# Kernel tuning notes

Hardware: AMD Instinct MI355X
Metric: run time of the kernel (lower is better)

The kernel has to match this reference:

```python
import jax, jax.numpy as jnp
import numpy as np

H, DST, DCONV, EXP = 640, 16, 4, 2
DIN = H * EXP          # 1280
DTR = -(-H // 16)      # 40
EPS = 1e-6


def rmsnorm(x, w):
    rms = jnp.sqrt(jnp.mean(x * x, axis=-1, keepdims=True) + EPS)
    return x / rms * w


def bitlinear(x, w, nw):
    # RMSNorm -> ternary weight quant + int8 activation quant (STE)
    x = rmsnorm(x, nw)
    alpha = jnp.maximum(jnp.mean(jnp.abs(w)), 1e-10)
    wq = jnp.clip(jnp.round(w / alpha), -1.0, 1.0)
    wq = w + jax.lax.stop_gradient(wq - w)
    gamma = jnp.maximum(jnp.max(jnp.abs(x), axis=-1, keepdims=True), 1e-10)
    xq = jnp.clip(jnp.round(x * 127.0 / gamma), -128.0, 127.0)
    xq = x + jax.lax.stop_gradient(xq - x)
    return (xq @ wq.T) * (alpha * gamma / 127.0)


def causal_conv1d(x, cw, cb):
    # x: [B,L,D]; depthwise causal conv, kernel DCONV
    pad = DCONV - 1
    xp = jnp.pad(x, ((0, 0), (pad, 0), (0, 0)))
    L = x.shape[1]
    out = jnp.zeros_like(x)
    for k in range(DCONV):
        out = out + xp[:, pad - k:pad - k + L, :] * cw[:, k]
    return out + cb


def selective_scan(x, dt, B_mat, C_mat, A_log):
    # x,dt: [B,L,D]; B_mat,C_mat: [B,L,N]; A_log: [D,N]
    A = -jnp.exp(A_log)
    dA = jnp.exp(A[None, None] * dt[..., None])                 # [B,L,D,N]
    dBx = dt[..., None] * B_mat[:, :, None, :] * x[..., None]   # [B,L,D,N]
    dA_t = jnp.moveaxis(dA, 1, 0)
    dBx_t = jnp.moveaxis(dBx, 1, 0)
    C_t = jnp.moveaxis(C_mat, 1, 0)

    def step(h, inp):
        da, dbx, c = inp
        h = da * h + dbx
        y = jnp.sum(h * c[:, None, :], axis=-1)  # [B,D]
        return h, y

    h0 = jnp.zeros(x.shape[:1] + (x.shape[2], A_log.shape[1]), x.dtype)
    _, ys = jax.lax.scan(step, h0, (dA_t, dBx_t, C_t))
    return jnp.moveaxis(ys, 0, 1)  # [B,L,D]


def setup_inputs() -> dict:
    key = jax.random.key(0)
    ks = jax.random.split(key, 10)
    sc_in = 1.0 / np.sqrt(H)
    sc_din = 1.0 / np.sqrt(DIN)
    A = np.tile(np.arange(1, DST + 1, dtype=np.float32)[None, :], (DIN, 1))
    return {
        "x": jax.random.normal(ks[0], (2, 2048, H), jnp.float32),
        "norm_w": jnp.ones((H,), jnp.float32),
        "in_w": jax.random.normal(ks[1], (DIN * 2, H), jnp.float32) * sc_in,
        "in_nw": jnp.ones((H,), jnp.float32),
        "conv_w": jax.random.normal(ks[2], (DIN, DCONV), jnp.float32) * 0.1,
        "conv_b": jnp.zeros((DIN,), jnp.float32),
        "dtu_w": jax.random.normal(ks[3], (DTR, DIN), jnp.float32) * sc_din,
        "dtu_nw": jnp.ones((DIN,), jnp.float32),
        "dtd_w": jax.random.normal(ks[4], (DIN, DTR), jnp.float32) / np.sqrt(DTR),
        "dtd_b": jnp.zeros((DIN,), jnp.float32),
        "Bp_w": jax.random.normal(ks[5], (DST, DIN), jnp.float32) * sc_din,
        "Bp_nw": jnp.ones((DIN,), jnp.float32),
        "Cp_w": jax.random.normal(ks[6], (DST, DIN), jnp.float32) * sc_din,
        "Cp_nw": jnp.ones((DIN,), jnp.float32),
        "A_log": jnp.asarray(np.log(A)),
        "D": jnp.ones((DIN,), jnp.float32),
        "out_w": jax.random.normal(ks[7], (H, DIN), jnp.float32) * sc_din,
        "out_nw": jnp.ones((DIN,), jnp.float32),
    }


def reference(x, norm_w, in_w, in_nw, conv_w, conv_b, dtu_w, dtu_nw, dtd_w, dtd_b,
              Bp_w, Bp_nw, Cp_w, Cp_nw, A_log, D, out_w, out_nw):
    residual = x
    xn = rmsnorm(x, norm_w)
    xz = bitlinear(xn, in_w, in_nw)
    x_path, z = jnp.split(xz, 2, axis=-1)
    x_path = causal_conv1d(x_path, conv_w, conv_b)
    x_path = jax.nn.silu(x_path)
    dt = jax.nn.softplus(bitlinear(x_path, dtu_w, dtu_nw) @ dtd_w.T + dtd_b)
    B_mat = bitlinear(x_path, Bp_w, Bp_nw)
    C_mat = bitlinear(x_path, Cp_w, Cp_nw)
    y = selective_scan(x_path, dt, B_mat, C_mat, A_log)
    y = y + x_path * D
    y = y * jax.nn.silu(z)
    return bitlinear(y, out_w, out_nw) + residual
```

## Files before the change

kernel.cpp:

```cpp
#include <hip/hip_runtime.h>
#include <hip/hip_bf16.h>
#include <cmath>

#define NROWS 4096
#define H_    640
#define DIN_  1280
#define DXZ   2560
#define DTR_  40
#define DST_  16
#define LSEQ  2048
#define EPS_  1e-6f
#define NCH   64
#define CL    32
#define NDG   20
#define KSPLIT 8
#define KCH (DIN_ / KSPLIT)
#define LOG2E 1.4426950408889634f
#define RLOG2E 0.6931471805599453f

typedef __attribute__((ext_vector_type(8))) short short8;
typedef __attribute__((ext_vector_type(4))) float f32x4;
typedef unsigned short ushort_t;

__device__ __forceinline__ float bf2f(short u) {
    return __uint_as_float((unsigned)(unsigned short)u << 16);
}
__device__ __forceinline__ short f2bfs(float x) { return (short)(__float_as_uint(x) >> 16); }

#define GLD16(gp, lp) __builtin_amdgcn_global_load_lds( \
    (const __attribute__((address_space(1))) unsigned int*)(unsigned long long)(gp), \
    (__attribute__((address_space(3))) unsigned int*)(unsigned int)(unsigned long long)(lp), 16, 0, 0)

__device__ __forceinline__ float wave_sum64(float v) {
    v += __shfl_xor(v, 1);  v += __shfl_xor(v, 2);  v += __shfl_xor(v, 4);
    v += __shfl_xor(v, 8);  v += __shfl_xor(v, 16); v += __shfl_xor(v, 32);
    return v;
}
__device__ __forceinline__ float wave_max64(float v) {
    v = fmaxf(v, __shfl_xor(v, 1));  v = fmaxf(v, __shfl_xor(v, 2));
    v = fmaxf(v, __shfl_xor(v, 4));  v = fmaxf(v, __shfl_xor(v, 8));
    v = fmaxf(v, __shfl_xor(v, 16)); v = fmaxf(v, __shfl_xor(v, 32));
    return v;
}
__device__ __forceinline__ float block_sum4(float v, float* red4) {
    v = wave_sum64(v);
    if ((threadIdx.x & 63) == 0) red4[threadIdx.x >> 6] = v;
    __syncthreads();
    return (red4[0] + red4[1]) + (red4[2] + red4[3]);
}
__device__ __forceinline__ float block_max4(float v, float* red4) {
    v = wave_max64(v);
    if ((threadIdx.x & 63) == 0) red4[threadIdx.x >> 6] = v;
    __syncthreads();
    return fmaxf(fmaxf(red4[0], red4[1]), fmaxf(red4[2], red4[3]));
}
__device__ __forceinline__ float block_reduce_sum256(float v, float* red) {
    int tid = threadIdx.x;
    red[tid] = v; __syncthreads();
    for (int o = 128; o; o >>= 1) { if (tid < o) red[tid] += red[tid + o]; __syncthreads(); }
    float r = red[0]; __syncthreads();
    return r;
}

__global__ __launch_bounds__(256) void k_pre(const float* __restrict__ x,
                                             const float* __restrict__ norm_w,
                                             const float* __restrict__ in_nw,
                                             const float* __restrict__ w0, const float* __restrict__ w1,
                                             const float* __restrict__ w2, const float* __restrict__ w3,
                                             const float* __restrict__ w4,
                                             int n0, int n1, int n2, int n3, int n4,
                                             __hip_bfloat16* __restrict__ xq, float* __restrict__ gamma,
                                             float* __restrict__ partials,
                                             float* __restrict__ zacc ) {
    __shared__ float red[256];
    const int tid = threadIdx.x;
    if (blockIdx.x < NROWS) {
        const int r = blockIdx.x;
        const float* xr = x + (size_t)r * H_;
        const bool has2 = (tid < H_ - 512);
        float v0 = xr[tid], v1 = xr[tid + 256], v2 = has2 ? xr[tid + 512] : 0.f;
        float sum = block_sum4(v0 * v0 + v1 * v1 + v2 * v2, red);
        float r1 = 1.f / sqrtf(sum / H_ + EPS_);
        v0 *= r1 * norm_w[tid];
        v1 *= r1 * norm_w[tid + 256];
        if (has2) v2 *= r1 * norm_w[tid + 512];
        sum = block_sum4(v0 * v0 + v1 * v1 + v2 * v2, red + 4);
        float r2 = 1.f / sqrtf(sum / H_ + EPS_);
        v0 *= r2 * in_nw[tid];
        v1 *= r2 * in_nw[tid + 256];
        if (has2) v2 *= r2 * in_nw[tid + 512];
        float mx = fmaxf(fmaxf(fabsf(v0), fabsf(v1)), fabsf(v2));
        float g = fmaxf(block_max4(mx, red + 8), 1e-10f);
        if (tid == 0) gamma[r] = g;
        float s = 127.f / g;
        __hip_bfloat16* o = xq + (size_t)r * H_;
        o[tid]       = __float2bfloat16(fminf(fmaxf(rintf(v0 * s), -128.f), 127.f));
        o[tid + 256] = __float2bfloat16(fminf(fmaxf(rintf(v1 * s), -128.f), 127.f));
        if (has2) o[tid + 512] = __float2bfloat16(fminf(fmaxf(rintf(v2 * s), -128.f), 127.f));
    } else {
        const int flat = blockIdx.x - NROWS;
        for (int i = flat * 256 + tid; i < NROWS * 72; i += 1280 * 256) zacc[i] = 0.f;
        const int wi = flat >> 8, xb = flat & 255;
        const float* w = (wi == 0) ? w0 : (wi == 1) ? w1 : (wi == 2) ? w2 : (wi == 3) ? w3 : w4;
        const int n = (wi == 0) ? n0 : (wi == 1) ? n1 : (wi == 2) ? n2 : (wi == 3) ? n3 : n4;
        float s = 0.f;
        for (int i = xb * 256 + tid; i < n; i += 65536) s += fabsf(w[i]);
        float t = block_reduce_sum256(s, red);
        if (tid == 0) partials[wi * 256 + xb] = t;
    }
}

__global__ __launch_bounds__(256) void k_quant_build(const float* __restrict__ in_w,
                                                     const float* __restrict__ out_w,
                                                     const float* __restrict__ dtu_w,
                                                     const float* __restrict__ Bp_w,
                                                     const float* __restrict__ Cp_w,
                                                     const float* __restrict__ partials,
                                                     float* __restrict__ alphas,
                                                     __hip_bfloat16* __restrict__ q_in,
                                                     __hip_bfloat16* __restrict__ q_out,
                                                     ushort_t* __restrict__ wq_sk,
                                                     int n0, int n1, int n2, int n3, int n4) {
    __shared__ double dred[256];
    const int tid = threadIdx.x;
    auto calc_alpha = [&](int wi, int n) -> float {
        double s = (double)partials[wi * 256 + tid];
        dred[tid] = s; __syncthreads();
        for (int o = 128; o; o >>= 1) { if (tid < o) dred[tid] += dred[tid + o]; __syncthreads(); }
        float a = fmaxf((float)(dred[0] / (double)n), 1e-10f);
        __syncthreads();
        return a;
    };
    if (blockIdx.x < 6400) {
        float a = calc_alpha(0, n0);
        if (blockIdx.x == 0) {
            float a1 = calc_alpha(1, n1), a2 = calc_alpha(2, n2);
            float a3 = calc_alpha(3, n3), a4 = calc_alpha(4, n4);
            if (tid == 0) {
                alphas[0] = a; alphas[1] = a1; alphas[2] = a2; alphas[3] = a3; alphas[4] = a4;
            }
        }
        int i = blockIdx.x * 256 + tid;
        ((ushort_t*)q_in)[i] = (ushort_t)f2bfs(fminf(fmaxf(rintf(in_w[i] / a), -1.f), 1.f));
    } else if (blockIdx.x < 9600) {
        float a = calc_alpha(4, n4);
        int i = (blockIdx.x - 6400) * 256 + tid;
        ((ushort_t*)q_out)[i] = (ushort_t)f2bfs(fminf(fmaxf(rintf(out_w[i] / a), -1.f), 1.f));
    } else {
        float a1 = calc_alpha(1, n1), a2 = calc_alpha(2, n2), a3 = calc_alpha(3, n3);
        int idx = (blockIdx.x - 9600) * 256 + tid;
        int t = idx / 2560, rem = idx % 2560, kb = rem / 64, l = rem % 64;
        int nloc = l & 15, kg = l >> 4;
        float alpha; const float* src; int row; bool valid = true;
        if (t < 3)      { alpha = a1; src = dtu_w; row = t * 16 + nloc; valid = (row < 40); }
        else if (t == 3){ alpha = a2; src = Bp_w;  row = nloc; }
        else            { alpha = a3; src = Cp_w;  row = nloc; }
        int k0 = kb * 32 + kg * 8;
        short8 outv;
#pragma unroll
        for (int e = 0; e < 8; ++e) {
            float q = valid ? fminf(fmaxf(rintf(src[(size_t)row * DIN_ + k0 + e] / alpha), -1.f), 1.f) : 0.f;
            outv[e] = f2bfs(q);
        }
        *(short8*)(wq_sk + (size_t)idx * 8) = outv;
    }
}

template<int BM, int BN>
__global__ __launch_bounds__(256) void k_gemm_mfma(const ushort_t* __restrict__ Aq,
                                                   const ushort_t* __restrict__ Wq,
                                                   const float* __restrict__ alpha_p,
                                                   const float* __restrict__ gamma,
                                                   const float* __restrict__ residual,
                                                   float* __restrict__ out,
                                                   int M, int N, int K) {
    constexpr int FM = BM / 32, FN = BN / 32;
    constexpr int NL = (BM + BN) / 64;
    __shared__ ushort_t As[3][BM * 32];
    __shared__ ushort_t Bs[3][BN * 32];
    const int tid = threadIdx.x;
    const int w = tid >> 6, lane = tid & 63;
    const int wm = w >> 1, wn = w & 1;
    const int nwg = gridDim.x * gridDim.y;
    const int hw = blockIdx.y * gridDim.x + blockIdx.x;
    const int work = (nwg % 8 == 0) ? ((hw & 7) * (nwg >> 3) + (hw >> 3)) : hw;
    const int row0 = (work / gridDim.x) * BM;
    const int col0 = (work % gridDim.x) * BN;
    f32x4 acc[FM][FN] = {};

    auto stage = [&](int buf, int k0) {
        #pragma unroll
        for (int q = 0; q < BM / 64; ++q) {
            int c = w * BM + q * 64 + lane;
            int row = c >> 2;
            int uslot = (c & 3) ^ (row & 3);
            GLD16(Aq + (size_t)(row0 + row) * K + k0 + uslot * 8,
                  (char*)As[buf] + (w * BM + q * 64) * 16);
        }
        #pragma unroll
        for (int q = 0; q < BN / 64; ++q) {
            int c = w * BN + q * 64 + lane;
            int row = c >> 2;
            int uslot = (c & 3) ^ (row & 3);
            GLD16(Wq + (size_t)(col0 + row) * K + k0 + uslot * 8,
                  (char*)Bs[buf] + (w * BN + q * 64) * 16);
        }
    };

    const int NT = K >> 5;
    stage(0, 0);
    if (NT > 1) stage(1, 32);
    int cur = 0;
    for (int t = 0; t < NT; ++t) {
        if (t + 2 < NT) {
            int nb = cur + 2; if (nb >= 3) nb -= 3;
            stage(nb, (t + 2) << 5);
            if constexpr (NL == 2)      asm volatile("s_waitcnt vmcnt(4)" ::: "memory");
            else if constexpr (NL == 3) asm volatile("s_waitcnt vmcnt(6)" ::: "memory");
            else                        asm volatile("s_waitcnt vmcnt(8)" ::: "memory");
        } else if (t + 1 < NT) {
            if constexpr (NL == 2)      asm volatile("s_waitcnt vmcnt(2)" ::: "memory");
            else if constexpr (NL == 3) asm volatile("s_waitcnt vmcnt(3)" ::: "memory");
            else                        asm volatile("s_waitcnt vmcnt(4)" ::: "memory");
        } else {
            asm volatile("s_waitcnt vmcnt(0)" ::: "memory");
        }
        __builtin_amdgcn_s_barrier();

        short8 a[FM], b[FN];
        #pragma unroll
        for (int i = 0; i < FM; ++i) {
            int row = wm * (BM / 2) + i * 16 + (lane & 15);
            int byt = row * 64 + (((lane >> 4) ^ (row & 3)) << 4);
            a[i] = *(const short8*)((const char*)As[cur] + byt);
        }
        #pragma unroll
        for (int j = 0; j < FN; ++j) {
            int row = wn * (BN / 2) + j * 16 + (lane & 15);
            int byt = row * 64 + (((lane >> 4) ^ (row & 3)) << 4);
            b[j] = *(const short8*)((const char*)Bs[cur] + byt);
        }
        #pragma unroll
        for (int i = 0; i < FM; ++i)
            #pragma unroll
            for (int j = 0; j < FN; ++j)
                acc[i][j] = __builtin_amdgcn_mfma_f32_16x16x32_bf16(a[i], b[j], acc[i][j], 0, 0, 0);
        asm volatile("" ::: "memory");
        __builtin_amdgcn_s_barrier();
        ++cur; if (cur == 3) cur = 0;
    }

    const float alpha = alpha_p[0];
    #pragma unroll
    for (int i = 0; i < FM; ++i) {
        #pragma unroll
        for (int r = 0; r < 4; ++r) {
            int row = row0 + wm * (BM / 2) + i * 16 + (lane >> 4) * 4 + r;
            float s = alpha * gamma[row] * (1.f / 127.f);
            #pragma unroll
            for (int j = 0; j < FN; ++j) {
                int col = col0 + wn * (BN / 2) + j * 16 + (lane & 15);
                float o = acc[i][j][r] * s;
                if (residual) o += residual[(size_t)row * N + col];
                out[(size_t)row * N + col] = o;
            }
        }
    }
}

__global__ __launch_bounds__(256) void k_conv_norm(const float* __restrict__ xz,
                                                   const float* __restrict__ cw, const float* __restrict__ cb,
                                                   const float* __restrict__ dtu_nw,
                                                   const float* __restrict__ Bp_nw,
                                                   const float* __restrict__ Cp_nw,
                                                   float* __restrict__ xp,
                                                   float* __restrict__ rinv_out, float* __restrict__ g3) {
    const int bb = blockIdx.x;
    const int row = ((bb & 7) << 9) | (bb >> 3);
    const int tid = threadIdx.x;
    const int l = row & (LSEQ - 1);
    __shared__ float red4[16];
    float vv[5];
    float ss = 0.f;
#pragma unroll
    for (int j = 0; j < 5; ++j) {
        int d = tid + j * 256;
        f32x4 c4 = *(const f32x4*)(cw + (size_t)d * 4);
        const float* base = xz + (size_t)row * DXZ + d;
        float s = cb[d] + base[0] * c4[0];
        if (l >= 1) s += base[-(ptrdiff_t)DXZ] * c4[1];
        if (l >= 2) s += base[-(ptrdiff_t)(2 * DXZ)] * c4[2];
        if (l >= 3) s += base[-(ptrdiff_t)(3 * DXZ)] * c4[3];
        float v = s / (1.f + __builtin_amdgcn_exp2f(-s * LOG2E));
        vv[j] = v;
        ss += v * v;
        xp[(size_t)row * DIN_ + d] = v;
    }
    float sum = block_sum4(ss, red4);
    float rms = 1.f / sqrtf(sum / DIN_ + EPS_);
    float m0 = 0.f, m1 = 0.f, m2 = 0.f;
#pragma unroll
    for (int j = 0; j < 5; ++j) {
        int d = tid + j * 256;
        float t = vv[j] * rms;
        m0 = fmaxf(m0, fabsf(t * dtu_nw[d]));
        m1 = fmaxf(m1, fabsf(t * Bp_nw[d]));
        m2 = fmaxf(m2, fabsf(t * Cp_nw[d]));
    }
    float g0 = block_max4(m0, red4 + 4);
    float g1 = block_max4(m1, red4 + 8);
    float g2 = block_max4(m2, red4 + 12);
    if (tid == 0) {
        rinv_out[row]       = rms;
        g3[row]             = fmaxf(g0, 1e-10f);
        g3[NROWS + row]     = fmaxf(g1, 1e-10f);
        g3[2 * NROWS + row] = fmaxf(g2, 1e-10f);
    }
}

__global__ __launch_bounds__(256) void k_skinny_mfma(const float* __restrict__ xp,
                                                     const float* __restrict__ rinv,
                                                     const float* __restrict__ dtu_nw,
                                                     const float* __restrict__ Bp_nw,
                                                     const float* __restrict__ Cp_nw,
                                                     const float* __restrict__ g3,
                                                     const ushort_t* __restrict__ wq_sk,
                                                     float* __restrict__ dtu_acc,
                                                     float* __restrict__ B_acc,
                                                     float* __restrict__ C_acc) {
    const int tid = threadIdx.x;
    const int w = tid >> 6, l = tid & 63;
    const int row0 = blockIdx.x * 64;
    const int kc0 = blockIdx.y * KCH;
    __shared__ float s_xp[64 * 36];
    __shared__ float s_nw[3 * KCH];
    for (int i = tid; i < 3 * KCH; i += 256) {
        int m = i / KCH, j = i - m * KCH;
        const float* nw = (m == 0) ? dtu_nw : (m == 1) ? Bp_nw : Cp_nw;
        s_nw[i] = nw[kc0 + j];
    }
    const int arow = row0 + w * 16 + (l & 15);
    const float ri = rinv[arow];
    const float s0 = 127.f / g3[arow];
    const float s1 = 127.f / g3[NROWS + arow];
    const float s2 = 127.f / g3[2 * NROWS + arow];
    const int kgrp = l >> 4;
    f32x4 acc[5] = {};

    for (int ks = 0; ks < KCH / 32; ++ks) {
        const int kc = kc0 + ks * 32;
        __syncthreads();
        {
            int srow = tid >> 2, scol = (tid & 3) * 8;
            const float* gp = xp + (size_t)(row0 + srow) * DIN_ + kc + scol;
            f32x4 u0 = *(const f32x4*)gp;
            f32x4 u1 = *(const f32x4*)(gp + 4);
            *(f32x4*)(s_xp + srow * 36 + scol)     = u0;
            *(f32x4*)(s_xp + srow * 36 + scol + 4) = u1;
        }
        __syncthreads();
        const float* sp = s_xp + (w * 16 + (l & 15)) * 36 + kgrp * 8;
        f32x4 t0 = *(const f32x4*)sp;
        f32x4 t1 = *(const f32x4*)(sp + 4);
        float t[8] = { t0[0]*ri, t0[1]*ri, t0[2]*ri, t0[3]*ri,
                       t1[0]*ri, t1[1]*ri, t1[2]*ri, t1[3]*ri };
        short8 a0, a1, a2;
        #pragma unroll
        for (int e = 0; e < 8; ++e) {
            int kk = ks * 32 + kgrp * 8 + e;
            float q0 = fminf(fmaxf(rintf(t[e] * s_nw[kk]           * s0), -128.f), 127.f);
            float q1 = fminf(fmaxf(rintf(t[e] * s_nw[KCH + kk]     * s1), -128.f), 127.f);
            float q2 = fminf(fmaxf(rintf(t[e] * s_nw[2 * KCH + kk] * s2), -128.f), 127.f);
            a0[e] = f2bfs(q0); a1[e] = f2bfs(q1); a2[e] = f2bfs(q2);
        }
        const int kbg = kc >> 5;
        short8 b0 = *(const short8*)(wq_sk + ((size_t)(0 * 40 + kbg) * 64 + l) * 8);
        short8 b1 = *(const short8*)(wq_sk + ((size_t)(1 * 40 + kbg) * 64 + l) * 8);
        short8 b2 = *(const short8*)(wq_sk + ((size_t)(2 * 40 + kbg) * 64 + l) * 8);
        short8 b3 = *(const short8*)(wq_sk + ((size_t)(3 * 40 + kbg) * 64 + l) * 8);
        short8 b4 = *(const short8*)(wq_sk + ((size_t)(4 * 40 + kbg) * 64 + l) * 8);
        acc[0] = __builtin_amdgcn_mfma_f32_16x16x32_bf16(a0, b0, acc[0], 0, 0, 0);
        acc[1] = __builtin_amdgcn_mfma_f32_16x16x32_bf16(a0, b1, acc[1], 0, 0, 0);
        acc[2] = __builtin_amdgcn_mfma_f32_16x16x32_bf16(a0, b2, acc[2], 0, 0, 0);
        acc[3] = __builtin_amdgcn_mfma_f32_16x16x32_bf16(a1, b3, acc[3], 0, 0, 0);
        acc[4] = __builtin_amdgcn_mfma_f32_16x16x32_bf16(a2, b4, acc[4], 0, 0, 0);
    }

    const int col = l & 15;
    const int rbase = row0 + w * 16 + (l >> 4) * 4;
    #pragma unroll
    for (int j = 0; j < 4; ++j) {
        int r = rbase + j;
        atomicAdd(&dtu_acc[(size_t)r * DTR_ + col],      acc[0][j]);
        atomicAdd(&dtu_acc[(size_t)r * DTR_ + 16 + col], acc[1][j]);
        if (col < 8) atomicAdd(&dtu_acc[(size_t)r * DTR_ + 32 + col], acc[2][j]);
        atomicAdd(&B_acc[(size_t)r * DST_ + col], acc[3][j]);
        atomicAdd(&C_acc[(size_t)r * DST_ + col], acc[4][j]);
    }
}

__global__ __launch_bounds__(256) void k_dtd(const float* __restrict__ U,
                                             const float* __restrict__ W,
                                             const float* __restrict__ bias,
                                             const float* __restrict__ g3,
                                             const float* __restrict__ alphas,
                                             float* __restrict__ dt) {
    const int c0 = blockIdx.x * 64;
    const int r0 = blockIdx.y * 32;
    const int tid = threadIdx.x;
    const int col = tid & 63, rg = tid >> 6;
    __shared__ float s_w[64 * 41];
    __shared__ float s_u[32 * 40];
    for (int i = tid; i < 64 * 40; i += 256) {
        int cc = i / 40, t = i - cc * 40;
        s_w[cc * 41 + t] = W[(size_t)c0 * 40 + i];
    }
    const float alpha = alphas[1];
    for (int i = tid; i < 32 * 40; i += 256) {
        int rr = i / 40;
        s_u[i] = ((U[(size_t)r0 * 40 + i] * alpha) * g3[r0 + rr]) * (1.f / 127.f);
    }
    __syncthreads();
    float w[40];
#pragma unroll
    for (int t = 0; t < 40; t++) w[t] = s_w[col * 41 + t];
    const float b = bias[c0 + col];
    for (int r8 = 0; r8 < 8; ++r8) {
        const int row = rg * 8 + r8;
        const float* ur = s_u + row * 40;
        float a0 = b, a1 = 0.f, a2 = 0.f, a3 = 0.f;
#pragma unroll
        for (int t = 0; t < 40; t += 4) {
            f32x4 uv = *(const f32x4*)(ur + t);
            a0 = fmaf(uv[0], w[t],     a0);
            a1 = fmaf(uv[1], w[t + 1], a1);
            a2 = fmaf(uv[2], w[t + 2], a2);
            a3 = fmaf(uv[3], w[t + 3], a3);
        }
        float s = (a0 + a1) + (a2 + a3);
        float e = __builtin_amdgcn_exp2f(-fabsf(s) * LOG2E);
        float sp = fmaxf(s, 0.f) + __builtin_amdgcn_logf(1.f + e) * RLOG2E;
        dt[(size_t)(r0 + row) * DIN_ + c0 + col] = sp;
    }
}

__global__ __launch_bounds__(256) void k_scan_a(const float* __restrict__ dt, const float* __restrict__ xp,
                                                const float* __restrict__ Bm, const float* __restrict__ A_log,
                                                const float* __restrict__ g3, const float* __restrict__ alphas,
                                                float* __restrict__ hloc, float* __restrict__ sdt_out) {
    const int tid = threadIdx.x;
    const int q = tid & 3, dloc = tid >> 2;
    const int dg = blockIdx.x, c = blockIdx.y, b = blockIdx.z;
    const int d = dg * 64 + dloc;
    const int l0 = c * CL;
    __shared__ float s_B[CL * 16];
    if (tid < CL * 4) {
        int rg = b * LSEQ + l0 + (tid >> 2);
        float a2 = alphas[2];
        float gB = g3[NROWS + rg];
        f32x4 Bv = *(const f32x4*)(Bm + (size_t)rg * DST_ + (tid & 3) * 4);
        f32x4 o;
#pragma unroll
        for (int k = 0; k < 4; ++k) o[k] = ((Bv[k] * a2) * gB) * (1.f / 127.f);
        *(f32x4*)(s_B + tid * 4) = o;
    }
    f32x4 Av = *(const f32x4*)(A_log + (size_t)d * DST_ + q * 4);
    float A2[4];
#pragma unroll
    for (int j = 0; j < 4; ++j) A2[j] = -expf(Av[j]) * LOG2E;
    __syncthreads();
    const float* dtp = dt + (size_t)(b * LSEQ + l0) * DIN_ + d;
    const float* xpp = xp + (size_t)(b * LSEQ + l0) * DIN_ + d;
    float h[4] = {};
    float sdt = 0.f;
    float dtv = *dtp, xv = *xpp;
    for (int l = 0; l < CL; ++l) {
        float ndt = 0.f, nx = 0.f;
        if (l + 1 < CL) { ndt = dtp[(size_t)(l + 1) * DIN_]; nx = xpp[(size_t)(l + 1) * DIN_]; }
        f32x4 Bv = *(const f32x4*)(s_B + l * 16 + q * 4);
        float dtx = dtv * xv;
        sdt += dtv;
#pragma unroll
        for (int j = 0; j < 4; ++j) {
            float dA = __builtin_amdgcn_exp2f(A2[j] * dtv);
            h[j] = fmaf(dA, h[j], Bv[j] * dtx);
        }
        dtv = ndt; xv = nx;
    }
    size_t base = ((size_t)(b * NDG + dg) * 64 + c) * 1024 + tid * 4;
    *(f32x4*)(hloc + base) = (f32x4){h[0], h[1], h[2], h[3]};
    if (q == 0) sdt_out[((size_t)(b * NDG + dg) * 64 + c) * 64 + dloc] = sdt;
}

__global__ __launch_bounds__(256) void k_scan_b(float* __restrict__ hloc, const float* __restrict__ sdt,
                                                const float* __restrict__ A_log) {
    const int tid = threadIdx.x;
    const int idx = blockIdx.x;
    const int b = idx / (NDG * 64);
    const int rem = idx % (NDG * 64);
    const int dg = rem / 64, dloc = rem % 64;
    const int d = dg * 64 + dloc;
    __shared__ float s_h[64 * 17];
    __shared__ float s_sdt[64];
    __shared__ float s_A2[16];
    const size_t gb = (size_t)(b * NDG + dg) * 64;
#pragma unroll
    for (int i = 0; i < 4; ++i) {
        int c = i * 16 + (tid >> 4), n = tid & 15;
        s_h[c * 17 + n] = hloc[(gb + c) * 1024 + dloc * 16 + n];
    }
    if (tid < 64) s_sdt[tid] = sdt[(gb + tid) * 64 + dloc];
    else if (tid < 80) s_A2[tid - 64] = -expf(A_log[(size_t)d * DST_ + (tid - 64)]) * LOG2E;
    __syncthreads();
    const int w = tid >> 6, lane = tid & 63;
#pragma unroll
    for (int nn = 0; nn < 4; ++nn) {
        int n = w * 4 + nn;
        float h = s_h[lane * 17 + n];
        float P = __builtin_amdgcn_exp2f(s_A2[n] * s_sdt[lane]);
#pragma unroll
        for (int s = 1; s < 64; s <<= 1) {
            float hp = __shfl_up(h, s);
            float Pp = __shfl_up(P, s);
            if (lane >= s) { h = fmaf(P, hp, h); P *= Pp; }
        }
        float Hi = __shfl_up(h, 1);
        if (lane == 0) Hi = 0.f;
        s_h[lane * 17 + n] = Hi;
    }
    __syncthreads();
#pragma unroll
    for (int i = 0; i < 4; ++i) {
        int c = i * 16 + (tid >> 4), n = tid & 15;
        hloc[(gb + c) * 1024 + dloc * 16 + n] = s_h[c * 17 + n];
    }
}

__global__ __launch_bounds__(256) void k_scan_c(const float* __restrict__ dt, const float* __restrict__ xp,
                                                const float* __restrict__ Bm, const float* __restrict__ Cm,
                                                const float* __restrict__ xz, const float* __restrict__ A_log,
                                                const float* __restrict__ Dvec, const float* __restrict__ g3,
                                                const float* __restrict__ alphas,
                                                const float* __restrict__ Hinit, float* __restrict__ y) {
    const int tid = threadIdx.x;
    const int q = tid & 3, dloc = tid >> 2;
    const int dg = blockIdx.x, c = blockIdx.y, b = blockIdx.z;
    const int d = dg * 64 + dloc;
    const int l0 = c * CL;
    __shared__ float s_B[CL * 16], s_C[CL * 16];
    if (tid < CL * 4) {
        int rg = b * LSEQ + l0 + (tid >> 2);
        float a2 = alphas[2];
        float gB = g3[NROWS + rg];
        f32x4 Bv = *(const f32x4*)(Bm + (size_t)rg * DST_ + (tid & 3) * 4);
        f32x4 o;
#pragma unroll
        for (int k = 0; k < 4; ++k) o[k] = ((Bv[k] * a2) * gB) * (1.f / 127.f);
        *(f32x4*)(s_B + tid * 4) = o;
    } else {
        int t2 = tid - CL * 4;
        int rg = b * LSEQ + l0 + (t2 >> 2);
        float a3 = alphas[3];
        float gC = g3[2 * NROWS + rg];
        f32x4 Cv = *(const f32x4*)(Cm + (size_t)rg * DST_ + (t2 & 3) * 4);
        f32x4 o;
#pragma unroll
        for (int k = 0; k < 4; ++k) o[k] = ((Cv[k] * a3) * gC) * (1.f / 127.f);
        *(f32x4*)(s_C + t2 * 4) = o;
    }
    f32x4 Av = *(const f32x4*)(A_log + (size_t)d * DST_ + q * 4);
    float A2[4];
#pragma unroll
    for (int j = 0; j < 4; ++j) A2[j] = -expf(Av[j]) * LOG2E;
    const float Dd = Dvec[d];
    __syncthreads();
    const float* dtp = dt + (size_t)(b * LSEQ + l0) * DIN_ + d;
    const float* xpp = xp + (size_t)(b * LSEQ + l0) * DIN_ + d;
    const float* zp  = xz + (size_t)(b * LSEQ + l0) * DXZ + DIN_ + d;
    float* yp = y + (size_t)(b * LSEQ + l0) * DIN_ + d;
    size_t base = ((size_t)(b * NDG + dg) * 64 + c) * 1024 + tid * 4;
    f32x4 hv = *(const f32x4*)(Hinit + base);
    float h[4] = {hv[0], hv[1], hv[2], hv[3]};
    float dtv = *dtp, xv = *xpp, zv = *zp;
    for (int l = 0; l < CL; ++l) {
        float ndt = 0.f, nx = 0.f, nz = 0.f;
        if (l + 1 < CL) {
            ndt = dtp[(size_t)(l + 1) * DIN_];
            nx  = xpp[(size_t)(l + 1) * DIN_];
            nz  = zp[(size_t)(l + 1) * DXZ];
        }
        f32x4 Bv = *(const f32x4*)(s_B + l * 16 + q * 4);
        f32x4 Cv = *(const f32x4*)(s_C + l * 16 + q * 4);
        float dtx = dtv * xv;
        float yv = 0.f;
#pragma unroll
        for (int j = 0; j < 4; ++j) {
            float dA = __builtin_amdgcn_exp2f(A2[j] * dtv);
            h[j] = fmaf(dA, h[j], Bv[j] * dtx);
            yv = fmaf(h[j], Cv[j], yv);
        }
        yv += __shfl_xor(yv, 1);
        yv += __shfl_xor(yv, 2);
        if (q == 0) {
            float sig = 1.f / (1.f + __builtin_amdgcn_exp2f(-zv * LOG2E));
            yp[(size_t)l * DIN_] = (yv + xv * Dd) * (zv * sig);
        }
        dtv = ndt; xv = nx; zv = nz;
    }
}

__global__ __launch_bounds__(256) void k_norm_y(const float* __restrict__ y,
                                                const float* __restrict__ out_nw,
                                                __hip_bfloat16* __restrict__ yq, float* __restrict__ gy) {
    const int r = blockIdx.x, tid = threadIdx.x;
    const float* yr = y + (size_t)r * DIN_;
    __shared__ float red4[8];
    float v[5];
    float ss = 0.f;
#pragma unroll
    for (int j = 0; j < 5; j++) { v[j] = yr[tid + j * 256]; ss += v[j] * v[j]; }
    float sum = block_sum4(ss, red4);
    float rms = 1.f / sqrtf(sum / DIN_ + EPS_);
    float mx = 0.f;
#pragma unroll
    for (int j = 0; j < 5; j++) {
        int i = tid + j * 256;
        v[j] = v[j] * rms * out_nw[i];
        mx = fmaxf(mx, fabsf(v[j]));
    }
    float g = fmaxf(block_max4(mx, red4 + 4), 1e-10f);
    if (tid == 0) gy[r] = g;
    float s = 127.f / g;
#pragma unroll
    for (int j = 0; j < 5; j++) {
        int i = tid + j * 256;
        yq[(size_t)r * DIN_ + i] = __float2bfloat16(fminf(fmaxf(rintf(v[j] * s), -128.f), 127.f));
    }
}

extern "C" void kernel_launch(void* const* d_in, const int* in_sizes, int n_in,
                              void* d_out, int out_size, void* d_ws, size_t ws_size,
                              hipStream_t stream) {
    (void)in_sizes; (void)n_in; (void)out_size;
    const float* x      = (const float*)d_in[0];
    const float* norm_w = (const float*)d_in[1];
    const float* in_w   = (const float*)d_in[2];
    const float* in_nw  = (const float*)d_in[3];
    const float* conv_w = (const float*)d_in[4];
    const float* conv_b = (const float*)d_in[5];
    const float* dtu_w  = (const float*)d_in[6];
    const float* dtu_nw = (const float*)d_in[7];
    const float* dtd_w  = (const float*)d_in[8];
    const float* dtd_b  = (const float*)d_in[9];
    const float* Bp_w   = (const float*)d_in[10];
    const float* Bp_nw  = (const float*)d_in[11];
    const float* Cp_w   = (const float*)d_in[12];
    const float* Cp_nw  = (const float*)d_in[13];
    const float* A_log  = (const float*)d_in[14];
    const float* Dv     = (const float*)d_in[15];
    const float* out_w  = (const float*)d_in[16];
    const float* out_nw = (const float*)d_in[17];

    float* ws = (float*)d_ws;
    float* alphas   = ws;
    float* partials = ws + 8;
    float* xq1      = ws + 8 + 5 * 256;
    float* gamma1   = xq1 + (size_t)NROWS * H_;
    float* xz       = gamma1 + NROWS;
    float* xp       = xz + (size_t)NROWS * DXZ;
    float* xpn     = xp + (size_t)NROWS * DIN_;
    float* g3       = xpn + (size_t)NROWS * DIN_;
    float* dtu_out  = g3 + 3 * NROWS;
    float* Bmat     = dtu_out + (size_t)NROWS * DTR_;
    float* Cmat     = Bmat + (size_t)NROWS * DST_;
    float* dtb      = Cmat + (size_t)NROWS * DST_;
    float* gy       = dtb + (size_t)NROWS * DIN_;
    float* wq_in    = gy + NROWS;
    float* wq_dtu   = wq_in + (size_t)DXZ * H_;
    float* wq_Bp    = wq_dtu + (size_t)DTR_ * DIN_;
    float* wq_Cp    = wq_Bp + (size_t)DST_ * DIN_;
    float* wq_out   = wq_Cp + (size_t)DST_ * DIN_;
    float* rinv     = wq_out + (size_t)H_ * DIN_;
    float* wq_sk    = rinv + NROWS;
    float* sdt      = wq_sk + 51200;
    size_t need = (size_t)((sdt + 2 * NDG * 64 * 64) - ws) * sizeof(float);
    if (ws_size < need) return;

    float* hloc = xq1;

    const int n0 = DXZ * H_, n1 = DTR_ * DIN_, n2 = DST_ * DIN_, n3 = DST_ * DIN_, n4 = H_ * DIN_;
    hipLaunchKernelGGL(k_pre, dim3(NROWS + 5 * 256), dim3(256), 0, stream,
                       x, norm_w, in_nw, in_w, dtu_w, Bp_w, Cp_w, out_w,
                       n0, n1, n2, n3, n4, (__hip_bfloat16*)xq1, gamma1, partials, dtu_out);
    hipLaunchKernelGGL(k_quant_build, dim3(9650), dim3(256), 0, stream,
                       in_w, out_w, dtu_w, Bp_w, Cp_w, partials, alphas,
                       (__hip_bfloat16*)wq_in, (__hip_bfloat16*)wq_out, (ushort_t*)wq_sk,
                       n0, n1, n2, n3, n4);

    hipLaunchKernelGGL((k_gemm_mfma<128, 128>), dim3(DXZ / 128, NROWS / 128), dim3(256), 0, stream,
                       (const ushort_t*)xq1, (const ushort_t*)wq_in, alphas + 0, gamma1,
                       (const float*)nullptr, xz, NROWS, DXZ, H_);
    hipLaunchKernelGGL(k_conv_norm, dim3(NROWS), dim3(256), 0, stream,
                       xz, conv_w, conv_b, dtu_nw, Bp_nw, Cp_nw, xp, rinv, g3);
    hipLaunchKernelGGL(k_skinny_mfma, dim3(NROWS / 64, KSPLIT), dim3(256), 0, stream,
                       xp, rinv, dtu_nw, Bp_nw, Cp_nw, g3, (const ushort_t*)wq_sk,
                       dtu_out, Bmat, Cmat);
    hipLaunchKernelGGL(k_dtd, dim3(DIN_ / 64, NROWS / 32), dim3(256), 0, stream,
                       dtu_out, dtd_w, dtd_b, g3, alphas, dtb);

    hipLaunchKernelGGL(k_scan_a, dim3(NDG, NCH, 2), dim3(256), 0, stream,
                       dtb, xp, Bmat, A_log, g3, alphas, hloc, sdt);
    hipLaunchKernelGGL(k_scan_b, dim3(2 * NDG * 64), dim3(256), 0, stream, hloc, sdt, A_log);
    hipLaunchKernelGGL(k_scan_c, dim3(NDG, NCH, 2), dim3(256), 0, stream,
                       dtb, xp, Bmat, Cmat, xz, A_log, Dv, g3, alphas, hloc, xpn );

    hipLaunchKernelGGL(k_norm_y, dim3(NROWS), dim3(256), 0, stream, xpn , out_nw,
                       (__hip_bfloat16*)dtb , gy);
    hipLaunchKernelGGL((k_gemm_mfma<64, 64>), dim3(H_ / 64, NROWS / 64), dim3(256), 0, stream,
                       (const ushort_t*)dtb , (const ushort_t*)wq_out, alphas + 4, gy,
                       x , (float*)d_out, NROWS, H_, DIN_);
}
```

Before: 223.6 us.

## Switch bitlinear GEMMs from bf16 MFMA to int8 MFMA with int8 operands

Quantized activations and ternary weights are now stored as int8 instead of bf16. The two large GEMMs use the i32 16x16x64 i8 MFMA with a K-step of 64 bytes per tile. This halves operand bytes moved from memory and through LDS, and raises MFMA throughput per instruction. The integer accumulation is exact for these value ranges, so results should be unchanged. Weights are requantized each call, as before.

```diff
diff --git a/kernel.cpp b/kernel.cpp
--- a/kernel.cpp
+++ b/kernel.cpp
@@ -20,7 +20,9 @@
 
 typedef __attribute__((ext_vector_type(8))) short short8;
 typedef __attribute__((ext_vector_type(4))) float f32x4;
+typedef __attribute__((ext_vector_type(4))) int i32x4;
 typedef unsigned short ushort_t;
+typedef signed char i8_t;
 
 __device__ __forceinline__ float bf2f(short u) {
     return __uint_as_float((unsigned)(unsigned short)u << 16);
@@ -69,7 +71,7 @@
                                              const float* __restrict__ w2, const float* __restrict__ w3,
                                              const float* __restrict__ w4,
                                              int n0, int n1, int n2, int n3, int n4,
-                                             __hip_bfloat16* __restrict__ xq, float* __restrict__ gamma,
+                                             i8_t* __restrict__ xq, float* __restrict__ gamma,
                                              float* __restrict__ partials,
                                              float* __restrict__ zacc ) {
     __shared__ float red[256];
@@ -93,10 +95,10 @@
         float g = fmaxf(block_max4(mx, red + 8), 1e-10f);
         if (tid == 0) gamma[r] = g;
         float s = 127.f / g;
-        __hip_bfloat16* o = xq + (size_t)r * H_;
-        o[tid]       = __float2bfloat16(fminf(fmaxf(rintf(v0 * s), -128.f), 127.f));
-        o[tid + 256] = __float2bfloat16(fminf(fmaxf(rintf(v1 * s), -128.f), 127.f));
-        if (has2) o[tid + 512] = __float2bfloat16(fminf(fmaxf(rintf(v2 * s), -128.f), 127.f));
+        i8_t* o = xq + (size_t)r * H_;
+        o[tid]       = (i8_t)(int)fminf(fmaxf(rintf(v0 * s), -128.f), 127.f);
+        o[tid + 256] = (i8_t)(int)fminf(fmaxf(rintf(v1 * s), -128.f), 127.f);
+        if (has2) o[tid + 512] = (i8_t)(int)fminf(fmaxf(rintf(v2 * s), -128.f), 127.f);
     } else {
         const int flat = blockIdx.x - NROWS;
         for (int i = flat * 256 + tid; i < NROWS * 72; i += 1280 * 256) zacc[i] = 0.f;
@@ -117,8 +119,8 @@
                                                      const float* __restrict__ Cp_w,
                                                      const float* __restrict__ partials,
                                                      float* __restrict__ alphas,
-                                                     __hip_bfloat16* __restrict__ q_in,
-                                                     __hip_bfloat16* __restrict__ q_out,
+                                                     i8_t* __restrict__ q_in,
+                                                     i8_t* __restrict__ q_out,
                                                      ushort_t* __restrict__ wq_sk,
                                                      int n0, int n1, int n2, int n3, int n4) {
     __shared__ double dred[256];
@@ -141,11 +143,11 @@
             }
         }
         int i = blockIdx.x * 256 + tid;
-        ((ushort_t*)q_in)[i] = (ushort_t)f2bfs(fminf(fmaxf(rintf(in_w[i] / a), -1.f), 1.f));
+        q_in[i] = (i8_t)(int)fminf(fmaxf(rintf(in_w[i] / a), -1.f), 1.f);
     } else if (blockIdx.x < 9600) {
         float a = calc_alpha(4, n4);
         int i = (blockIdx.x - 6400) * 256 + tid;
-        ((ushort_t*)q_out)[i] = (ushort_t)f2bfs(fminf(fmaxf(rintf(out_w[i] / a), -1.f), 1.f));
+        q_out[i] = (i8_t)(int)fminf(fmaxf(rintf(out_w[i] / a), -1.f), 1.f);
     } else {
         float a1 = calc_alpha(1, n1), a2 = calc_alpha(2, n2), a3 = calc_alpha(3, n3);
         int idx = (blockIdx.x - 9600) * 256 + tid;
@@ -167,17 +169,17 @@
 }
 
 template<int BM, int BN>
-__global__ __launch_bounds__(256) void k_gemm_mfma(const ushort_t* __restrict__ Aq,
-                                                   const ushort_t* __restrict__ Wq,
-                                                   const float* __restrict__ alpha_p,
-                                                   const float* __restrict__ gamma,
-                                                   const float* __restrict__ residual,
-                                                   float* __restrict__ out,
-                                                   int M, int N, int K) {
+__global__ __launch_bounds__(256) void k_gemm_i8(const i8_t* __restrict__ Aq,
+                                                 const i8_t* __restrict__ Wq,
+                                                 const float* __restrict__ alpha_p,
+                                                 const float* __restrict__ gamma,
+                                                 const float* __restrict__ residual,
+                                                 float* __restrict__ out,
+                                                 int M, int N, int K) {
     constexpr int FM = BM / 32, FN = BN / 32;
     constexpr int NL = (BM + BN) / 64;
-    __shared__ ushort_t As[3][BM * 32];
-    __shared__ ushort_t Bs[3][BN * 32];
+    __shared__ i8_t As[3][BM * 64];
+    __shared__ i8_t Bs[3][BN * 64];
     const int tid = threadIdx.x;
     const int w = tid >> 6, lane = tid & 63;
     const int wm = w >> 1, wn = w & 1;
@@ -186,7 +188,7 @@
     const int work = (nwg % 8 == 0) ? ((hw & 7) * (nwg >> 3) + (hw >> 3)) : hw;
     const int row0 = (work / gridDim.x) * BM;
     const int col0 = (work % gridDim.x) * BN;
-    f32x4 acc[FM][FN] = {};
+    i32x4 acc[FM][FN] = {};
 
     auto stage = [&](int buf, int k0) {
         #pragma unroll
@@ -194,7 +196,7 @@
             int c = w * BM + q * 64 + lane;
             int row = c >> 2;
             int uslot = (c & 3) ^ (row & 3);
-            GLD16(Aq + (size_t)(row0 + row) * K + k0 + uslot * 8,
+            GLD16(Aq + (size_t)(row0 + row) * K + k0 + uslot * 16,
                   (char*)As[buf] + (w * BM + q * 64) * 16);
         }
         #pragma unroll
@@ -202,19 +204,19 @@
             int c = w * BN + q * 64 + lane;
             int row = c >> 2;
             int uslot = (c & 3) ^ (row & 3);
-            GLD16(Wq + (size_t)(col0 + row) * K + k0 + uslot * 8,
+            GLD16(Wq + (size_t)(col0 + row) * K + k0 + uslot * 16,
                   (char*)Bs[buf] + (w * BN + q * 64) * 16);
         }
     };
 
-    const int NT = K >> 5;
+    const int NT = K >> 6;
     stage(0, 0);
-    if (NT > 1) stage(1, 32);
+    if (NT > 1) stage(1, 64);
     int cur = 0;
     for (int t = 0; t < NT; ++t) {
         if (t + 2 < NT) {
             int nb = cur + 2; if (nb >= 3) nb -= 3;
-            stage(nb, (t + 2) << 5);
+            stage(nb, (t + 2) << 6);
             if constexpr (NL == 2)      asm volatile("s_waitcnt vmcnt(4)" ::: "memory");
             else if constexpr (NL == 3) asm volatile("s_waitcnt vmcnt(6)" ::: "memory");
             else                        asm volatile("s_waitcnt vmcnt(8)" ::: "memory");
@@ -227,24 +229,24 @@
         }
         __builtin_amdgcn_s_barrier();
 
-        short8 a[FM], b[FN];
+        i32x4 a[FM], b[FN];
         #pragma unroll
         for (int i = 0; i < FM; ++i) {
             int row = wm * (BM / 2) + i * 16 + (lane & 15);
             int byt = row * 64 + (((lane >> 4) ^ (row & 3)) << 4);
-            a[i] = *(const short8*)((const char*)As[cur] + byt);
+            a[i] = *(const i32x4*)((const char*)As[cur] + byt);
         }
         #pragma unroll
         for (int j = 0; j < FN; ++j) {
             int row = wn * (BN / 2) + j * 16 + (lane & 15);
             int byt = row * 64 + (((lane >> 4) ^ (row & 3)) << 4);
-            b[j] = *(const short8*)((const char*)Bs[cur] + byt);
+            b[j] = *(const i32x4*)((const char*)Bs[cur] + byt);
         }
         #pragma unroll
         for (int i = 0; i < FM; ++i)
             #pragma unroll
             for (int j = 0; j < FN; ++j)
-                acc[i][j] = __builtin_amdgcn_mfma_f32_16x16x32_bf16(a[i], b[j], acc[i][j], 0, 0, 0);
+                acc[i][j] = __builtin_amdgcn_mfma_i32_16x16x64_i8(a[i], b[j], acc[i][j], 0, 0, 0);
         asm volatile("" ::: "memory");
         __builtin_amdgcn_s_barrier();
         ++cur; if (cur == 3) cur = 0;
@@ -260,7 +262,7 @@
             #pragma unroll
             for (int j = 0; j < FN; ++j) {
                 int col = col0 + wn * (BN / 2) + j * 16 + (lane & 15);
-                float o = acc[i][j][r] * s;
+                float o = (float)acc[i][j][r] * s;
                 if (residual) o += residual[(size_t)row * N + col];
                 out[(size_t)row * N + col] = o;
             }
@@ -611,7 +613,7 @@
 
 __global__ __launch_bounds__(256) void k_norm_y(const float* __restrict__ y,
                                                 const float* __restrict__ out_nw,
-                                                __hip_bfloat16* __restrict__ yq, float* __restrict__ gy) {
+                                                i8_t* __restrict__ yq, float* __restrict__ gy) {
     const int r = blockIdx.x, tid = threadIdx.x;
     const float* yr = y + (size_t)r * DIN_;
     __shared__ float red4[8];
@@ -634,7 +636,7 @@
 #pragma unroll
     for (int j = 0; j < 5; j++) {
         int i = tid + j * 256;
-        yq[(size_t)r * DIN_ + i] = __float2bfloat16(fminf(fmaxf(rintf(v[j] * s), -128.f), 127.f));
+        yq[(size_t)r * DIN_ + i] = (i8_t)(int)fminf(fmaxf(rintf(v[j] * s), -128.f), 127.f);
     }
 }
 
@@ -691,14 +693,14 @@
     const int n0 = DXZ * H_, n1 = DTR_ * DIN_, n2 = DST_ * DIN_, n3 = DST_ * DIN_, n4 = H_ * DIN_;
     hipLaunchKernelGGL(k_pre, dim3(NROWS + 5 * 256), dim3(256), 0, stream,
                        x, norm_w, in_nw, in_w, dtu_w, Bp_w, Cp_w, out_w,
-                       n0, n1, n2, n3, n4, (__hip_bfloat16*)xq1, gamma1, partials, dtu_out);
+                       n0, n1, n2, n3, n4, (i8_t*)xq1, gamma1, partials, dtu_out);
     hipLaunchKernelGGL(k_quant_build, dim3(9650), dim3(256), 0, stream,
                        in_w, out_w, dtu_w, Bp_w, Cp_w, partials, alphas,
-                       (__hip_bfloat16*)wq_in, (__hip_bfloat16*)wq_out, (ushort_t*)wq_sk,
+                       (i8_t*)wq_in, (i8_t*)wq_out, (ushort_t*)wq_sk,
                        n0, n1, n2, n3, n4);
 
-    hipLaunchKernelGGL((k_gemm_mfma<128, 128>), dim3(DXZ / 128, NROWS / 128), dim3(256), 0, stream,
-                       (const ushort_t*)xq1, (const ushort_t*)wq_in, alphas + 0, gamma1,
+    hipLaunchKernelGGL((k_gemm_i8<128, 128>), dim3(DXZ / 128, NROWS / 128), dim3(256), 0, stream,
+                       (const i8_t*)xq1, (const i8_t*)wq_in, alphas + 0, gamma1,
                        (const float*)nullptr, xz, NROWS, DXZ, H_);
     hipLaunchKernelGGL(k_conv_norm, dim3(NROWS), dim3(256), 0, stream,
                        xz, conv_w, conv_b, dtu_nw, Bp_nw, Cp_nw, xp, rinv, g3);
@@ -715,8 +717,8 @@
                        dtb, xp, Bmat, Cmat, xz, A_log, Dv, g3, alphas, hloc, xpn );
 
     hipLaunchKernelGGL(k_norm_y, dim3(NROWS), dim3(256), 0, stream, xpn , out_nw,
-                       (__hip_bfloat16*)dtb , gy);
-    hipLaunchKernelGGL((k_gemm_mfma<64, 64>), dim3(H_ / 64, NROWS / 64), dim3(256), 0, stream,
-                       (const ushort_t*)dtb , (const ushort_t*)wq_out, alphas + 4, gy,
+                       (i8_t*)dtb , gy);
+    hipLaunchKernelGGL((k_gemm_i8<64, 64>), dim3(H_ / 64, NROWS / 64), dim3(256), 0, stream,
+                       (const i8_t*)dtb , (const i8_t*)wq_out, alphas + 4, gy,
                        x , (float*)d_out, NROWS, H_, DIN_);
 }
```

New measurement: 200.1 us (median of 3 runs). 10.5% less time.
